# Kernel optimization log

Hardware: AMD Instinct MI355X
Metric: run time of the kernel (lower is better)

The kernel has to match this reference:

```python
import jax, jax.numpy as jnp
import numpy as np

B, N, E = 16, 5000, 40000
IN_DIM, HID, GRU_OUT = 128, 512, 16
G0, G1, G2 = 1, 128, 128          # gcn_dim = [1,128,128]
M0, M1, M2 = 512, 1024, N * GRU_OUT  # gru_out_linear MLP dims (hidden_num prepended)
EPS = 1e-5                         # BatchNorm1d eps (eval: running mean 0, var 1)


def _gcn_norm(edge_index, n):
    loop = jnp.arange(n)
    src = jnp.concatenate([edge_index[0], loop])
    dst = jnp.concatenate([edge_index[1], loop])
    deg = jax.ops.segment_sum(jnp.ones(src.shape[0], jnp.float32), dst, num_segments=n)
    dinv = 1.0 / jnp.sqrt(deg)
    return src, dst, dinv[src] * dinv[dst]


def _gcn_conv(h, W, b, src, dst, norm):
    hw = jnp.einsum('bnf,fg->bng', h, W)
    msgs = hw[:, src, :] * norm[None, :, None]            # [B,E+N,Fout]
    agg = jax.ops.segment_sum(jnp.swapaxes(msgs, 0, 1), dst, num_segments=h.shape[1])
    return jnp.swapaxes(agg, 0, 1) + b


def _gru_cell(x, h, Wih, Whh, bih, bhh):
    gi = x @ Wih.T + bih
    gh = h @ Whh.T + bhh
    ir, iz, ig = jnp.split(gi, 3, axis=-1)
    hr, hz, hg = jnp.split(gh, 3, axis=-1)
    r = jax.nn.sigmoid(ir + hr)
    z = jax.nn.sigmoid(iz + hz)
    n = jnp.tanh(ig + r * hg)
    return (1.0 - z) * n + z * h


def _mlp_block(x, W, b, a, g, be):
    # Dropout(eval)=Identity -> Linear -> PReLU -> BatchNorm1d(eval, rm=0, rv=1)
    y = x @ W.T + b
    y = jnp.where(y >= 0, y, a * y)
    return y / jnp.sqrt(1.0 + EPS) * g + be


def setup_inputs():
    key = jax.random.key(0)
    ks = jax.random.split(key, 32)
    f = lambda i, shp, s=0.02: jax.random.normal(ks[i], shp, jnp.float32) * s
    return dict(
        x=jax.random.normal(ks[0], (B, IN_DIM), jnp.float32),
        smoothed_vert_pos=jax.random.normal(ks[1], (B, N * 3), jnp.float32),
        edge_index=jax.random.randint(ks[2], (2, E), 0, N),
        Wih=f(3, (3 * HID, IN_DIM)), Whh=f(4, (3 * HID, HID)),
        bih=f(5, (3 * HID,)), bhh=f(6, (3 * HID,)),
        Wg1=f(7, (G0, G1), 0.1), bg1=f(8, (G1,)),
        Wg2=f(9, (G1, G2), 0.1), bg2=f(10, (G2,)),
        W1=f(11, (M1, M0)), b1=f(12, (M1,)),
        a1=jnp.full((M1,), 0.25, jnp.float32),
        g1=1.0 + f(13, (M1,)), be1=f(14, (M1,)),
        W2=f(15, (M2, M1), 0.01), b2=f(16, (M2,)),
        a2=jnp.full((M2,), 0.25, jnp.float32),
        g2=1.0 + f(17, (M2,)), be2=f(18, (M2,)),
        Wo=f(19, (1, G2 + GRU_OUT)), bo=f(20, (1,)),
    )


def reference(x, smoothed_vert_pos, edge_index, Wih, Whh, bih, bhh,
              Wg1, bg1, Wg2, bg2, W1, b1, a1, g1, be1,
              W2, b2, a2, g2, be2, Wo, bo):
    b = x.shape[0]
    svp = smoothed_vert_pos.reshape(b, N, 3)
    src, dst, norm = _gcn_norm(edge_index, N)
    z = svp[:, :, 2:3]                                   # channel j+2, j=0
    h1 = _gcn_conv(z, Wg1, bg1, src, dst, norm)          # [B,N,G1], no nonlinearity between convs (as in source)
    res = _gcn_conv(h1, Wg2, bg2, src, dst, norm)        # [B,N,G2]
    hidden = jnp.zeros((b, HID), x.dtype)                # hidden=None path
    next_hidden = _gru_cell(x, hidden, Wih, Whh, bih, bhh)
    m = _mlp_block(next_hidden, W1, b1, a1, g1, be1)
    m = _mlp_block(m, W2, b2, a2, g2, be2)
    gru_out = m.reshape(b, N, GRU_OUT)
    y = jnp.concatenate([gru_out, res], axis=2) @ Wo.T + bo  # [B,N,1]
    return y.reshape(b, N), next_hidden
```

## Files before the change

### kernel.cpp

```cpp
#include <hip/hip_runtime.h>
#include <hip/hip_bf16.h>

#define NN 5000
#define BB 16
#define EE 40000
#define INF 128
#define HID 512
#define M1D 1024
#define EPSV 1e-5f

typedef float f4 __attribute__((ext_vector_type(4)));

__device__ __forceinline__ float dot4(f4 a, f4 b) {
    return fmaf(a.x, b.x, fmaf(a.y, b.y, fmaf(a.z, b.z, a.w * b.w)));
}
__device__ __forceinline__ f4 ntload(const float* p) {
    return __builtin_nontemporal_load((const f4*)p);
}
__device__ __forceinline__ float dpp_xor1(float x) {
    return __int_as_float(__builtin_amdgcn_update_dpp(0, __float_as_int(x), 0xB1, 0xF, 0xF, true));
}
__device__ __forceinline__ float dpp_xor2(float x) {
    return __int_as_float(__builtin_amdgcn_update_dpp(0, __float_as_int(x), 0x4E, 0xF, 0xF, true));
}
__device__ __forceinline__ float dpp_xor8(float x) {
    return __int_as_float(__builtin_amdgcn_update_dpp(0, __float_as_int(x), 0x128, 0xF, 0xF, true));
}

#define GRU_BLOCKS 128
#define DEG_BLOCKS 157
#define ZPACK_BLOCKS 313
#define ZERO_BLOCKS 157

__global__ __launch_bounds__(256)
void k_s1(const int* __restrict__ ei, const float* __restrict__ x,
          const float* __restrict__ svp,
          const float* __restrict__ Wih, const float* __restrict__ bih,
          const float* __restrict__ bhh,
          const float* __restrict__ Wg1, const float* __restrict__ bg1,
          const float* __restrict__ Wg2, const float* __restrict__ bg2,
          const float* __restrict__ Wo, const float* __restrict__ bo,
          float* __restrict__ deg, float* __restrict__ nh,
          float* __restrict__ outNH, float* __restrict__ cst,
          float* __restrict__ zpack, float* __restrict__ zerobase) {
    const int blk = blockIdx.x;
    const int tid = threadIdx.x;

    if (blk < GRU_BLOCKS) {
        const int t = blk * 256 + tid;
        const int q = t & 3, idx = t >> 2;
        const int b = idx >> 9, h = idx & 511;
        const float* xb = x + b * INF;
        const float* wr = Wih + (size_t)h * INF;
        const float* wz = Wih + (size_t)(HID + h) * INF;
        const float* wg = Wih + (size_t)(2 * HID + h) * INF;
        float ir = 0.f, iz = 0.f, ig = 0.f;
        #pragma unroll 8
        for (int i = 0; i < 8; ++i) {
            const int k0 = i * 16 + q * 4;
            const f4 xv = *(const f4*)(xb + k0);
            ir += dot4(xv, *(const f4*)(wr + k0));
            iz += dot4(xv, *(const f4*)(wz + k0));
            ig += dot4(xv, *(const f4*)(wg + k0));
        }
        ir += __shfl_xor(ir, 1); ir += __shfl_xor(ir, 2);
        iz += __shfl_xor(iz, 1); iz += __shfl_xor(iz, 2);
        ig += __shfl_xor(ig, 1); ig += __shfl_xor(ig, 2);
        if (q == 0) {
            ir += bih[h]; iz += bih[HID + h]; ig += bih[2 * HID + h];
            float r  = 1.f / (1.f + expf(-(ir + bhh[h])));
            float z  = 1.f / (1.f + expf(-(iz + bhh[HID + h])));
            float nv = tanhf(ig + r * bhh[2 * HID + h]);
            float v  = (1.f - z) * nv;
            nh[idx] = v;
            outNH[idx] = v;
        }
    } else if (blk < GRU_BLOCKS + DEG_BLOCKS) {
        const int e = (blk - GRU_BLOCKS) * 256 + tid;
        if (e < EE) atomicAdd(&deg[ei[EE + e]], 1.0f);
    } else if (blk == GRU_BLOCKS + DEG_BLOCKS) {
        __shared__ float su[128], sv[128], sc[128];
        const int g = tid;
        if (g < 128) {
            float t = 0.f;
            for (int c = 0; c < 128; ++c) t = fmaf(Wg2[g * 128 + c], Wo[16 + c], t);
            su[g] = Wg1[g] * t;
            sv[g] = bg1[g] * t;
            sc[g] = bg2[g] * Wo[16 + g];
        }
        __syncthreads();
        for (int s = 64; s > 0; s >>= 1) {
            if (g < s) { su[g] += su[g + s]; sv[g] += sv[g + s]; sc[g] += sc[g + s]; }
            __syncthreads();
        }
        if (g == 0) { cst[0] = su[0]; cst[1] = sv[0]; cst[2] = sc[0] + bo[0]; }
    } else if (blk < GRU_BLOCKS + DEG_BLOCKS + 1 + ZPACK_BLOCKS) {
        const int t = (blk - (GRU_BLOCKS + DEG_BLOCKS + 1)) * 256 + tid;
        if (t < NN * BB) {
            const int n = t >> 4, b = t & 15;
            zpack[t] = svp[b * (NN * 3) + 3 * n + 2];
        }
    } else {
        const int t = (blk - (GRU_BLOCKS + DEG_BLOCKS + 1 + ZPACK_BLOCKS)) * 256 + tid;
        if (t < 2 * BB * NN / 4) ((f4*)zerobase)[t] = (f4)(0.f);
    }
}

#define AGG1_BLOCKS 2500
#define MLP_BLOCKS 256

__global__ __launch_bounds__(256)
void k_s2(const int* __restrict__ ei, const float* __restrict__ deg,
          const float* __restrict__ zpack, const float* __restrict__ nh,
          const float* __restrict__ W1, const float* __restrict__ b1,
          const float* __restrict__ a1, const float* __restrict__ g1,
          const float* __restrict__ be1,
          float* __restrict__ m1, float* __restrict__ aggzE, float* __restrict__ s1E) {
    const int blk = blockIdx.x;
    const int tid = threadIdx.x;

    if (blk < AGG1_BLOCKS) {
        const int t = blk * 256 + tid;
        const int e = t >> 4, b = t & 15;
        const int s = ei[e], d = ei[EE + e];
        const float w = rsqrtf(1.f + deg[s]) * rsqrtf(1.f + deg[d]);
        atomicAdd(&aggzE[d * 16 + b], w * zpack[s * 16 + b]);
        if (b == 0) atomicAdd(&s1E[d], w);
    } else {
        const int t = (blk - AGG1_BLOCKS) * 256 + tid;
        const int q = t & 3, idx = t >> 2;
        const int b = idx >> 10, i = idx & 1023;
        const float* hb = nh + b * HID;
        const float* wr = W1 + (size_t)i * HID;
        float acc = 0.f;
        #pragma unroll 8
        for (int ii = 0; ii < 32; ++ii) {
            const int k0 = ii * 16 + q * 4;
            acc += dot4(*(const f4*)(hb + k0), *(const f4*)(wr + k0));
        }
        acc += __shfl_xor(acc, 1); acc += __shfl_xor(acc, 2);
        if (q == 0) {
            acc += b1[i];
            float v = acc >= 0.f ? acc : a1[i] * acc;
            m1[idx] = v * (1.f / sqrtf(1.f + EPSV)) * g1[i] + be1[i];
        }
    }
}

#define BIG_BLOCKS 1000
#define AGG2_BLOCKS 2500

__global__ __launch_bounds__(256, 4)
void k_s3(const float* __restrict__ W2, const float* __restrict__ m1,
          const float* __restrict__ b2, const float* __restrict__ a2,
          const float* __restrict__ g2, const float* __restrict__ be2,
          const float* __restrict__ Wo,
          const int* __restrict__ ei, const float* __restrict__ deg,
          const float* __restrict__ zpack, const float* __restrict__ aggzE,
          float* __restrict__ aggz2E, float* __restrict__ ysum) {
    __shared__ float accs[4][80][16];
    const int blk = blockIdx.x;
    const int tid = threadIdx.x;

    if (blk < BIG_BLOCKS) {
        const int w = tid >> 6, l = tid & 63;
        const int koff = w * 256 + l * 4;
        const int n0 = blk * 5;
        const int jbase = n0 * 16;

        float4 m1r[16];
        #pragma unroll
        for (int b = 0; b < 16; ++b)
            m1r[b] = *(const float4*)(m1 + b * M1D + koff);

        const int hi0 = l & 1, hi1 = (l >> 1) & 1, hi2 = (l >> 2) & 1, hi3 = (l >> 3) & 1;
        const int brev = ((l & 1) << 3) | ((l & 2) << 1) | ((l & 4) >> 1) | ((l & 8) >> 3);

        const float* wp = W2 + (size_t)jbase * M1D + koff;
        f4 w0 = ntload(wp);
        f4 w1 = ntload(wp + M1D);
        f4 w2v = ntload(wp + 2 * M1D);
        for (int jj = 0; jj < 80; ++jj) {
            const int jn = (jj + 3 < 80) ? (jj + 3) : 79;
            const f4 wn = ntload(wp + (size_t)jn * M1D);
            float acc[16];
            #pragma unroll
            for (int b = 0; b < 16; ++b)
                acc[b] = fmaf(w0.x, m1r[b].x, fmaf(w0.y, m1r[b].y,
                         fmaf(w0.z, m1r[b].z, w0.w * m1r[b].w)));
            float r8[8];
            #pragma unroll
            for (int i = 0; i < 8; ++i) {
                float keep = hi0 ? acc[8 + i] : acc[i];
                float send = hi0 ? acc[i]     : acc[8 + i];
                r8[i] = keep + dpp_xor1(send);
            }
            float r4[4];
            #pragma unroll
            for (int i = 0; i < 4; ++i) {
                float keep = hi1 ? r8[4 + i] : r8[i];
                float send = hi1 ? r8[i]     : r8[4 + i];
                r4[i] = keep + dpp_xor2(send);
            }
            float r2[2];
            #pragma unroll
            for (int i = 0; i < 2; ++i) {
                float keep = hi2 ? r4[2 + i] : r4[i];
                float send = hi2 ? r4[i]     : r4[2 + i];
                r2[i] = keep + __shfl_xor(send, 4, 64);
            }
            float keep = hi3 ? r2[1] : r2[0];
            float send = hi3 ? r2[0] : r2[1];
            float r1 = keep + dpp_xor8(send);
            r1 += __shfl_xor(r1, 16, 64);
            r1 += __shfl_xor(r1, 32, 64);
            if (l < 16) accs[w][jj][brev] = r1;
            w0 = w1; w1 = w2v; w2v = wn;
        }
        __syncthreads();

        if (tid < 80) {
            const int nl = tid >> 4, b = tid & 15;
            const float invs = 1.f / sqrtf(1.f + EPSV);
            float sum = 0.f;
            #pragma unroll
            for (int kk = 0; kk < 16; ++kk) {
                const int rloc = nl * 16 + kk;
                const int j = jbase + rloc;
                float a = accs[0][rloc][b] + accs[1][rloc][b]
                        + accs[2][rloc][b] + accs[3][rloc][b] + b2[j];
                float v = a >= 0.f ? a : a2[j] * a;
                float val = v * invs * g2[j] + be2[j];
                sum = fmaf(val, Wo[kk], sum);
            }
            ysum[n0 * 16 + tid] = sum;
        }
    } else {
        const int t = (blk - BIG_BLOCKS) * 256 + tid;
        const int e = t >> 4, b = t & 15;
        const int s = ei[e], d = ei[EE + e];
        const float degs = deg[s];
        const float d2s = 1.f / (1.f + degs);
        const float w = rsqrtf(1.f + degs) * rsqrtf(1.f + deg[d]);
        const float A1s = aggzE[s * 16 + b] + d2s * zpack[s * 16 + b];
        atomicAdd(&aggz2E[d * 16 + b], w * A1s);
    }
}

__global__ __launch_bounds__(256)
void k_fin(const float* __restrict__ ysum, const float* __restrict__ aggzE,
           const float* __restrict__ aggz2E, const float* __restrict__ s1E,
           const float* __restrict__ deg, const float* __restrict__ zpack,
           const float* __restrict__ cst, float* __restrict__ y) {
    const int t = blockIdx.x * 256 + threadIdx.x;
    if (t >= BB * NN) return;
    const int n = t >> 4, b = t & 15;
    const float U = cst[0], V = cst[1], C0 = cst[2];
    const float d2 = 1.f / (1.f + deg[n]);
    const float z  = zpack[t];
    const float A1 = aggzE[t] + d2 * z;
    const float A2 = aggz2E[t] + d2 * A1;
    const float S1v = s1E[n] + d2;
    y[b * NN + n] = ysum[t] + U * A2 + V * S1v + C0;
}


extern "C" void kernel_launch(void* const* d_in, const int* in_sizes, int n_in,
                              void* d_out, int out_size, void* d_ws, size_t ws_size,
                              hipStream_t stream) {
    const float* x   = (const float*)d_in[0];
    const float* svp = (const float*)d_in[1];
    const int*   ei  = (const int*)d_in[2];
    const float* Wih = (const float*)d_in[3];
    const float* bih = (const float*)d_in[5];
    const float* bhh = (const float*)d_in[6];
    const float* Wg1 = (const float*)d_in[7];
    const float* bg1 = (const float*)d_in[8];
    const float* Wg2 = (const float*)d_in[9];
    const float* bg2 = (const float*)d_in[10];
    const float* W1  = (const float*)d_in[11];
    const float* b1  = (const float*)d_in[12];
    const float* a1  = (const float*)d_in[13];
    const float* g1  = (const float*)d_in[14];
    const float* be1 = (const float*)d_in[15];
    const float* W2  = (const float*)d_in[16];
    const float* b2  = (const float*)d_in[17];
    const float* a2  = (const float*)d_in[18];
    const float* g2  = (const float*)d_in[19];
    const float* be2 = (const float*)d_in[20];
    const float* Wo  = (const float*)d_in[21];
    const float* bo  = (const float*)d_in[22];
    float* out = (float*)d_out;

    float* ws      = (float*)d_ws;
    float* deg     = ws;
    float* s1E     = deg + NN;
    float* aggzE   = s1E + NN;
    float* aggz2E  = aggzE + BB * NN;
    float* zpack   = aggz2E + BB * NN;
    float* ysum    = zpack + BB * NN;
    float* nh      = ysum + BB * NN;
    float* m1      = nh + BB * HID;
    float* cst     = m1 + BB * M1D;

    hipMemsetAsync(ws, 0, (size_t)(2 * NN) * sizeof(float), stream);

    k_s1<<<dim3(GRU_BLOCKS + DEG_BLOCKS + 1 + ZPACK_BLOCKS + ZERO_BLOCKS),
           dim3(256), 0, stream>>>(
        ei, x, svp, Wih, bih, bhh, Wg1, bg1, Wg2, bg2, Wo, bo,
        deg, nh, out + BB * NN, cst, zpack, aggzE );

    k_s2<<<dim3(AGG1_BLOCKS + MLP_BLOCKS), dim3(256), 0, stream>>>(
        ei, deg, zpack, nh, W1, b1, a1, g1, be1, m1, aggzE, s1E);

    k_s3<<<dim3(BIG_BLOCKS + AGG2_BLOCKS), dim3(256), 0, stream>>>(
        W2, m1, b2, a2, g2, be2, Wo, ei, deg, zpack, aggzE, aggz2E, ysum);

    k_fin<<<dim3((BB * NN + 255) / 256), dim3(256), 0, stream>>>(
        ysum, aggzE, aggz2E, s1E, deg, zpack, cst, out);
}
```

Before: 106.4 us.

## Fold edge-aggregation work into GEMV blocks and coarsen scatter blocks

In k_s3 the separate 2500 edge-scatter blocks are removed. Each of the 1000 W2 GEMV blocks now first handles 640 edge-batch items of the second GCN aggregation before streaming its weights. In k_s2 the MLP blocks are moved to the front and the first aggregation is coarsened to 744 blocks of 861 items each. The aim is to cut block-launch and tail overhead and overlap atomic scatter latency with the memory-bound GEMV. The cost is that each GEMV block is serialized behind its atomic work, which could lengthen the critical path.

After: 107.9 us. No clear change (+1.4%).

```diff
diff --git a/kernel.cpp b/kernel.cpp
--- a/kernel.cpp
+++ b/kernel.cpp
@@ -106,8 +106,9 @@
     }
 }
 
-#define AGG1_BLOCKS 2500
 #define MLP_BLOCKS 256
+#define AGG1_BLOCKS 744
+#define AGG1_PER_BLOCK 861
 
 __global__ __launch_bounds__(256)
 void k_s2(const int* __restrict__ ei, const float* __restrict__ deg,
@@ -119,15 +120,8 @@
     const int blk = blockIdx.x;
     const int tid = threadIdx.x;
 
-    if (blk < AGG1_BLOCKS) {
+    if (blk < MLP_BLOCKS) {
         const int t = blk * 256 + tid;
-        const int e = t >> 4, b = t & 15;
-        const int s = ei[e], d = ei[EE + e];
-        const float w = rsqrtf(1.f + deg[s]) * rsqrtf(1.f + deg[d]);
-        atomicAdd(&aggzE[d * 16 + b], w * zpack[s * 16 + b]);
-        if (b == 0) atomicAdd(&s1E[d], w);
-    } else {
-        const int t = (blk - AGG1_BLOCKS) * 256 + tid;
         const int q = t & 3, idx = t >> 2;
         const int b = idx >> 10, i = idx & 1023;
         const float* hb = nh + b * HID;
@@ -144,11 +138,27 @@
             float v = acc >= 0.f ? acc : a1[i] * acc;
             m1[idx] = v * (1.f / sqrtf(1.f + EPSV)) * g1[i] + be1[i];
         }
+    } else {
+        const int base = (blk - MLP_BLOCKS) * AGG1_PER_BLOCK;
+        #pragma unroll
+        for (int i = 0; i < 4; ++i) {
+            const int it = i * 256 + tid;
+            if (it < AGG1_PER_BLOCK) {
+                const int t = base + it;
+                if (t < EE * BB) {
+                    const int e = t >> 4, b = t & 15;
+                    const int s = ei[e], d = ei[EE + e];
+                    const float w = rsqrtf(1.f + deg[s]) * rsqrtf(1.f + deg[d]);
+                    atomicAdd(&aggzE[d * 16 + b], w * zpack[s * 16 + b]);
+                    if (b == 0) atomicAdd(&s1E[d], w);
+                }
+            }
+        }
     }
 }
 
 #define BIG_BLOCKS 1000
-#define AGG2_BLOCKS 2500
+#define AGG2_PER_BLOCK 640
 
 __global__ __launch_bounds__(256, 4)
 void k_s3(const float* __restrict__ W2, const float* __restrict__ m1,
@@ -162,88 +172,95 @@
     const int blk = blockIdx.x;
     const int tid = threadIdx.x;
 
-    if (blk < BIG_BLOCKS) {
-        const int w = tid >> 6, l = tid & 63;
-        const int koff = w * 256 + l * 4;
-        const int n0 = blk * 5;
-        const int jbase = n0 * 16;
-
-        float4 m1r[16];
+    {
+        const int base = blk * AGG2_PER_BLOCK;
+        #pragma unroll
+        for (int i = 0; i < 3; ++i) {
+            const int it = i * 256 + tid;
+            if (it < AGG2_PER_BLOCK) {
+                const int t = base + it;
+                const int e = t >> 4, b = t & 15;
+                const int s = ei[e], d = ei[EE + e];
+                const float degs = deg[s];
+                const float d2s = 1.f / (1.f + degs);
+                const float w = rsqrtf(1.f + degs) * rsqrtf(1.f + deg[d]);
+                const float A1s = aggzE[s * 16 + b] + d2s * zpack[s * 16 + b];
+                atomicAdd(&aggz2E[d * 16 + b], w * A1s);
+            }
+        }
+    }
+
+    const int w = tid >> 6, l = tid & 63;
+    const int koff = w * 256 + l * 4;
+    const int n0 = blk * 5;
+    const int jbase = n0 * 16;
+
+    float4 m1r[16];
+    #pragma unroll
+    for (int b = 0; b < 16; ++b)
+        m1r[b] = *(const float4*)(m1 + b * M1D + koff);
+
+    const int hi0 = l & 1, hi1 = (l >> 1) & 1, hi2 = (l >> 2) & 1, hi3 = (l >> 3) & 1;
+    const int brev = ((l & 1) << 3) | ((l & 2) << 1) | ((l & 4) >> 1) | ((l & 8) >> 3);
+
+    const float* wp = W2 + (size_t)jbase * M1D + koff;
+    f4 w0 = ntload(wp);
+    f4 w1 = ntload(wp + M1D);
+    f4 w2v = ntload(wp + 2 * M1D);
+    for (int jj = 0; jj < 80; ++jj) {
+        const int jn = (jj + 3 < 80) ? (jj + 3) : 79;
+        const f4 wn = ntload(wp + (size_t)jn * M1D);
+        float acc[16];
         #pragma unroll
         for (int b = 0; b < 16; ++b)
-            m1r[b] = *(const float4*)(m1 + b * M1D + koff);
-
-        const int hi0 = l & 1, hi1 = (l >> 1) & 1, hi2 = (l >> 2) & 1, hi3 = (l >> 3) & 1;
-        const int brev = ((l & 1) << 3) | ((l & 2) << 1) | ((l & 4) >> 1) | ((l & 8) >> 3);
-
-        const float* wp = W2 + (size_t)jbase * M1D + koff;
-        f4 w0 = ntload(wp);
-        f4 w1 = ntload(wp + M1D);
-        f4 w2v = ntload(wp + 2 * M1D);
-        for (int jj = 0; jj < 80; ++jj) {
-            const int jn = (jj + 3 < 80) ? (jj + 3) : 79;
-            const f4 wn = ntload(wp + (size_t)jn * M1D);
-            float acc[16];
-            #pragma unroll
-            for (int b = 0; b < 16; ++b)
-                acc[b] = fmaf(w0.x, m1r[b].x, fmaf(w0.y, m1r[b].y,
-                         fmaf(w0.z, m1r[b].z, w0.w * m1r[b].w)));
-            float r8[8];
-            #pragma unroll
-            for (int i = 0; i < 8; ++i) {
-                float keep = hi0 ? acc[8 + i] : acc[i];
-                float send = hi0 ? acc[i]     : acc[8 + i];
-                r8[i] = keep + dpp_xor1(send);
-            }
-            float r4[4];
-            #pragma unroll
-            for (int i = 0; i < 4; ++i) {
-                float keep = hi1 ? r8[4 + i] : r8[i];
-                float send = hi1 ? r8[i]     : r8[4 + i];
-                r4[i] = keep + dpp_xor2(send);
-            }
-            float r2[2];
-            #pragma unroll
-            for (int i = 0; i < 2; ++i) {
-                float keep = hi2 ? r4[2 + i] : r4[i];
-                float send = hi2 ? r4[i]     : r4[2 + i];
-                r2[i] = keep + __shfl_xor(send, 4, 64);
-            }
-            float keep = hi3 ? r2[1] : r2[0];
-            float send = hi3 ? r2[0] : r2[1];
-            float r1 = keep + dpp_xor8(send);
-            r1 += __shfl_xor(r1, 16, 64);
-            r1 += __shfl_xor(r1, 32, 64);
-            if (l < 16) accs[w][jj][brev] = r1;
-            w0 = w1; w1 = w2v; w2v = wn;
-        }
-        __syncthreads();
-
-        if (tid < 80) {
-            const int nl = tid >> 4, b = tid & 15;
-            const float invs = 1.f / sqrtf(1.f + EPSV);
-            float sum = 0.f;
-            #pragma unroll
-            for (int kk = 0; kk < 16; ++kk) {
-                const int rloc = nl * 16 + kk;
-                const int j = jbase + rloc;
-                float a = accs[0][rloc][b] + accs[1][rloc][b]
-                        + accs[2][rloc][b] + accs[3][rloc][b] + b2[j];
-                float v = a >= 0.f ? a : a2[j] * a;
-                float val = v * invs * g2[j] + be2[j];
-                sum = fmaf(val, Wo[kk], sum);
-            }
-            ysum[n0 * 16 + tid] = sum;
-        }
-    } else {
-        const int t = (blk - BIG_BLOCKS) * 256 + tid;
-        const int e = t >> 4, b = t & 15;
-        const int s = ei[e], d = ei[EE + e];
-        const float degs = deg[s];
-        const float d2s = 1.f / (1.f + degs);
-        const float w = rsqrtf(1.f + degs) * rsqrtf(1.f + deg[d]);
-        const float A1s = aggzE[s * 16 + b] + d2s * zpack[s * 16 + b];
-        atomicAdd(&aggz2E[d * 16 + b], w * A1s);
+            acc[b] = fmaf(w0.x, m1r[b].x, fmaf(w0.y, m1r[b].y,
+                     fmaf(w0.z, m1r[b].z, w0.w * m1r[b].w)));
+        float r8[8];
+        #pragma unroll
+        for (int i = 0; i < 8; ++i) {
+            float keep = hi0 ? acc[8 + i] : acc[i];
+            float send = hi0 ? acc[i]     : acc[8 + i];
+            r8[i] = keep + dpp_xor1(send);
+        }
+        float r4[4];
+        #pragma unroll
+        for (int i = 0; i < 4; ++i) {
+            float keep = hi1 ? r8[4 + i] : r8[i];
+            float send = hi1 ? r8[i]     : r8[4 + i];
+            r4[i] = keep + dpp_xor2(send);
+        }
+        float r2[2];
+        #pragma unroll
+        for (int i = 0; i < 2; ++i) {
+            float keep = hi2 ? r4[2 + i] : r4[i];
+            float send = hi2 ? r4[i]     : r4[2 + i];
+            r2[i] = keep + __shfl_xor(send, 4, 64);
+        }
+        float keep = hi3 ? r2[1] : r2[0];
+        float send = hi3 ? r2[0] : r2[1];
+        float r1 = keep + dpp_xor8(send);
+        r1 += __shfl_xor(r1, 16, 64);
+        r1 += __shfl_xor(r1, 32, 64);
+        if (l < 16) accs[w][jj][brev] = r1;
+        w0 = w1; w1 = w2v; w2v = wn;
+    }
+    __syncthreads();
+
+    if (tid < 80) {
+        const int nl = tid >> 4, b = tid & 15;
+        const float invs = 1.f / sqrtf(1.f + EPSV);
+        float sum = 0.f;
+        #pragma unroll
+        for (int kk = 0; kk < 16; ++kk) {
+            const int rloc = nl * 16 + kk;
+            const int j = jbase + rloc;
+            float a = accs[0][rloc][b] + accs[1][rloc][b]
+                    + accs[2][rloc][b] + accs[3][rloc][b] + b2[j];
+            float v = a >= 0.f ? a : a2[j] * a;
+            float val = v * invs * g2[j] + be2[j];
+            sum = fmaf(val, Wo[kk], sum);
+        }
+        ysum[n0 * 16 + tid] = sum;
     }
 }
 
@@ -310,10 +327,10 @@
         ei, x, svp, Wih, bih, bhh, Wg1, bg1, Wg2, bg2, Wo, bo,
         deg, nh, out + BB * NN, cst, zpack, aggzE );
 
-    k_s2<<<dim3(AGG1_BLOCKS + MLP_BLOCKS), dim3(256), 0, stream>>>(
+    k_s2<<<dim3(MLP_BLOCKS + AGG1_BLOCKS), dim3(256), 0, stream>>>(
         ei, deg, zpack, nh, W1, b1, a1, g1, be1, m1, aggzE, s1E);
 
-    k_s3<<<dim3(BIG_BLOCKS + AGG2_BLOCKS), dim3(256), 0, stream>>>(
+    k_s3<<<dim3(BIG_BLOCKS), dim3(256), 0, stream>>>(
         W2, m1, b2, a2, g2, be2, Wo, ei, deg, zpack, aggzE, aggz2E, ysum);
 
     k_fin<<<dim3((BB * NN + 255) / 256), dim3(256), 0, stream>>>(
```
